# Optimization experiments

Hardware: AMD Instinct MI355X
Metric: run time of the kernel (lower is better)

## Reference

```python
import jax, jax.numpy as jnp
import numpy as np

M_STAGES = 10  # log2(1024)

def butterfly_mult_untied(twiddle, x, increasing_stride=True):
    """twiddle: (nstack, m, n//2, 2, 2); x: (batch, n) -> (batch, nstack*n)."""
    b, n = x.shape
    nstack, m = twiddle.shape[0], twiddle.shape[1]
    out = jnp.broadcast_to(x[:, None, :], (b, nstack, n))
    for block in range(m):
        log_stride = block if increasing_stride else (m - 1 - block)
        stride = 1 << log_stride
        # twiddle[:, log_stride] stores the factor for this stride
        t = twiddle[:, log_stride].reshape(nstack, n // (2 * stride), stride, 2, 2)
        o = out.reshape(b, nstack, n // (2 * stride), 2, stride)
        # new[b,k,g,i,s] = sum_j t[k,g,s,i,j] * o[b,k,g,j,s]
        out = jnp.einsum('kgsij,bkgjs->bkgis', t, o).reshape(b, nstack, n)
    return out.reshape(b, nstack * n)

def setup_inputs() -> dict:
    key = jax.random.key(0)
    k1, k2, k3 = jax.random.split(key, 3)
    in_size = 1024
    batch = 32768
    nstack = 1
    x = jax.random.normal(k1, (batch, in_size), dtype=jnp.float32)
    # non-ortho init: randn / sqrt(2)
    twiddle = jax.random.normal(k2, (nstack, M_STAGES, in_size // 2, 2, 2), dtype=jnp.float32) / np.sqrt(2.0).astype(np.float32)
    bound = 1.0 / np.sqrt(in_size)
    bias = jax.random.uniform(k3, (in_size,), dtype=jnp.float32, minval=-bound, maxval=bound)
    return {"x": x, "twiddle": twiddle, "bias": bias}

def reference(x, twiddle, bias):
    # in_size == in_size_extended == out_size (power of 2): no pad / mean / slice branches
    out = butterfly_mult_untied(twiddle, x, increasing_stride=True)
    return out + bias
```

## Files before the change

### kernel.cpp

```cpp
#include <hip/hip_runtime.h>


constexpr int ROWS  = 4;
constexpr int WAVES = 4;
constexpr int N     = 1024;

__device__ __forceinline__ void pair_update(float (&v)[ROWS][16], int s0, int s1,
                                            const float4 t4)
{
    #pragma unroll
    for (int r = 0; r < ROWS; ++r) {
        const float x0 = v[r][s0], x1 = v[r][s1];
        v[r][s0] = t4.x * x0 + t4.y * x1;
        v[r][s1] = t4.z * x0 + t4.w * x1;
    }
}

template<int LS>
__device__ __forceinline__ void cross_stage(float (&v)[ROWS][16],
                                            const float* __restrict__ tw,
                                            int lane)
{
    constexpr int m = 1 << (LS - 2);
    const int ipos = (lane >> (LS - 2)) & 1;
    const float* __restrict__ base = tw + LS * 2048;
    #pragma unroll
    for (int i = 0; i < 4; ++i) {
        #pragma unroll
        for (int j = 0; j < 4; ++j) {
            const int e    = i * 256 + lane * 4 + j;
            const int pair = ((e >> (LS + 1)) << LS) | (e & ((1 << LS) - 1));
            const float2 t2 = *reinterpret_cast<const float2*>(
                base + (size_t)pair * 4 + ipos * 2);
            const float ta = ipos ? t2.y : t2.x;
            const float tb = ipos ? t2.x : t2.y;
            const int s = i * 4 + j;
            #pragma unroll
            for (int r = 0; r < ROWS; ++r) {
                const float own  = v[r][s];
                const float part = __shfl_xor(own, m, 64);
                v[r][s] = ta * own + tb * part;
            }
        }
    }
}

__global__ __launch_bounds__(WAVES * 64)
void butterfly_kernel(const float* __restrict__ x,
                      const float* __restrict__ tw,
                      const float* __restrict__ bias,
                      float* __restrict__ out,
                      int batch)
{
    const int lane = (int)(threadIdx.x & 63u);
    const int wave = (int)(threadIdx.x >> 6u);
    const int row0 = (blockIdx.x * WAVES + wave) * ROWS;
    if (row0 >= batch) return;

    float v[ROWS][16];

    #pragma unroll
    for (int r = 0; r < ROWS; ++r) {
        const int row = (row0 + r < batch) ? (row0 + r) : (batch - 1);
        const float4* __restrict__ src =
            reinterpret_cast<const float4*>(x + (size_t)row * N);
        #pragma unroll
        for (int i = 0; i < 4; ++i) {
            const float4 t = src[i * 64 + lane];
            v[r][i*4+0] = t.x; v[r][i*4+1] = t.y;
            v[r][i*4+2] = t.z; v[r][i*4+3] = t.w;
        }
    }

    #pragma unroll
    for (int i = 0; i < 4; ++i) {
        #pragma unroll
        for (int jj = 0; jj < 2; ++jj) {
            const int pair = i * 128 + lane * 2 + jj;
            const float4 t4 = *reinterpret_cast<const float4*>(tw + (size_t)pair * 4);
            pair_update(v, i*4 + jj*2, i*4 + jj*2 + 1, t4);
        }
    }

    #pragma unroll
    for (int i = 0; i < 4; ++i) {
        #pragma unroll
        for (int j = 0; j < 2; ++j) {
            const int pair = i * 128 + lane * 2 + j;
            const float4 t4 = *reinterpret_cast<const float4*>(tw + 2048 + (size_t)pair * 4);
            pair_update(v, i*4 + j, i*4 + j + 2, t4);
        }
    }

    cross_stage<2>(v, tw, lane);
    cross_stage<3>(v, tw, lane);
    cross_stage<4>(v, tw, lane);
    cross_stage<5>(v, tw, lane);
    cross_stage<6>(v, tw, lane);
    cross_stage<7>(v, tw, lane);

    #pragma unroll
    for (int ih = 0; ih < 2; ++ih) {
        #pragma unroll
        for (int j = 0; j < 4; ++j) {
            const int pair = ih * 256 + lane * 4 + j;
            const float4 t4 = *reinterpret_cast<const float4*>(tw + 8*2048 + (size_t)pair * 4);
            pair_update(v, ih*8 + j, ih*8 + 4 + j, t4);
        }
    }

    #pragma unroll
    for (int i = 0; i < 2; ++i) {
        #pragma unroll
        for (int j = 0; j < 4; ++j) {
            const int pair = i * 256 + lane * 4 + j;
            const float4 t4 = *reinterpret_cast<const float4*>(tw + 9*2048 + (size_t)pair * 4);
            pair_update(v, i*4 + j, i*4 + 8 + j, t4);
        }
    }

    #pragma unroll
    for (int i = 0; i < 4; ++i) {
        const float4 b4 = *reinterpret_cast<const float4*>(bias + i * 256 + lane * 4);
        #pragma unroll
        for (int r = 0; r < ROWS; ++r) {
            if (row0 + r < batch) {
                float4 o;
                o.x = v[r][i*4+0] + b4.x;
                o.y = v[r][i*4+1] + b4.y;
                o.z = v[r][i*4+2] + b4.z;
                o.w = v[r][i*4+3] + b4.w;
                *reinterpret_cast<float4*>(out + (size_t)(row0 + r) * N + i * 256 + lane * 4) = o;
            }
        }
    }
}

extern "C" void kernel_launch(void* const* d_in, const int* in_sizes, int n_in,
                              void* d_out, int out_size, void* d_ws, size_t ws_size,
                              hipStream_t stream)
{
    (void)n_in; (void)d_ws; (void)ws_size; (void)out_size;
    const float* x    = (const float*)d_in[0];
    const float* tw   = (const float*)d_in[1];
    const float* bias = (const float*)d_in[2];
    float* out        = (float*)d_out;

    const int batch = in_sizes[0] / N;
    const int rows_per_block = WAVES * ROWS;
    const int blocks = (batch + rows_per_block - 1) / rows_per_block;
    hipLaunchKernelGGL(butterfly_kernel, dim3(blocks), dim3(WAVES * 64), 0, stream,
                       x, tw, bias, out, batch);
}
```

Before: 79.47 us.

## Transpose tile so each lane owns 64 contiguous columns of one row

Restructures the butterfly kernel so 1024-thread blocks process 64 rows, with each lane holding 64 consecutive columns of one row after an LDS transpose. The first six stages run fully in registers with wave-uniform (scalar) twiddle loads, and the last four stages exchange data between waves through swizzled LDS instead of lane shuffles. The aim is to remove the many cross-lane shuffles and per-lane twiddle gathers of the old layout. In exchange it adds many block-wide barriers, 64 KB of shared memory per block that limits occupancy, and heavy register pressure from 64 floats per thread.

After: 241.0 us. 203% more time.

```diff
diff --git a/kernel.cpp b/kernel.cpp
--- a/kernel.cpp
+++ b/kernel.cpp
@@ -1,137 +1,138 @@
 #include <hip/hip_runtime.h>
 
 
-constexpr int ROWS  = 4;
-constexpr int WAVES = 4;
-constexpr int N     = 1024;
+constexpr int N  = 1024;
+constexpr int TR = 64;
 
-__device__ __forceinline__ void pair_update(float (&v)[ROWS][16], int s0, int s1,
-                                            const float4 t4)
-{
-    #pragma unroll
-    for (int r = 0; r < ROWS; ++r) {
-        const float x0 = v[r][s0], x1 = v[r][s1];
-        v[r][s0] = t4.x * x0 + t4.y * x1;
-        v[r][s1] = t4.z * x0 + t4.w * x1;
-    }
-}
-
-template<int LS>
-__device__ __forceinline__ void cross_stage(float (&v)[ROWS][16],
-                                            const float* __restrict__ tw,
-                                            int lane)
-{
-    constexpr int m = 1 << (LS - 2);
-    const int ipos = (lane >> (LS - 2)) & 1;
-    const float* __restrict__ base = tw + LS * 2048;
-    #pragma unroll
-    for (int i = 0; i < 4; ++i) {
-        #pragma unroll
-        for (int j = 0; j < 4; ++j) {
-            const int e    = i * 256 + lane * 4 + j;
-            const int pair = ((e >> (LS + 1)) << LS) | (e & ((1 << LS) - 1));
-            const float2 t2 = *reinterpret_cast<const float2*>(
-                base + (size_t)pair * 4 + ipos * 2);
-            const float ta = ipos ? t2.y : t2.x;
-            const float tb = ipos ? t2.x : t2.y;
-            const int s = i * 4 + j;
-            #pragma unroll
-            for (int r = 0; r < ROWS; ++r) {
-                const float own  = v[r][s];
-                const float part = __shfl_xor(own, m, 64);
-                v[r][s] = ta * own + tb * part;
-            }
-        }
-    }
-}
-
-__global__ __launch_bounds__(WAVES * 64)
+__global__ __launch_bounds__(1024)
 void butterfly_kernel(const float* __restrict__ x,
                       const float* __restrict__ tw,
                       const float* __restrict__ bias,
                       float* __restrict__ out,
                       int batch)
 {
-    const int lane = (int)(threadIdx.x & 63u);
-    const int wave = (int)(threadIdx.x >> 6u);
-    const int row0 = (blockIdx.x * WAVES + wave) * ROWS;
-    if (row0 >= batch) return;
+    __shared__ __align__(16) float lds[16384];
 
-    float v[ROWS][16];
+    const int tid = (int)threadIdx.x;
+    const int l   = tid & 63;
+    const int w   = tid >> 6;
+    const int wu  = __builtin_amdgcn_readfirstlane(w);
+    const int row0 = (int)blockIdx.x * TR;
 
-    #pragma unroll
-    for (int r = 0; r < ROWS; ++r) {
-        const int row = (row0 + r < batch) ? (row0 + r) : (batch - 1);
-        const float4* __restrict__ src =
-            reinterpret_cast<const float4*>(x + (size_t)row * N);
+    float v[64];
+    float4* const ex = reinterpret_cast<float4*>(lds);
+
+    float4 tmp[4];
+    {
         #pragma unroll
-        for (int i = 0; i < 4; ++i) {
-            const float4 t = src[i * 64 + lane];
-            v[r][i*4+0] = t.x; v[r][i*4+1] = t.y;
-            v[r][i*4+2] = t.z; v[r][i*4+3] = t.w;
+        for (int kk = 0; kk < 4; ++kk) {
+            const int R = w * 4 + kk;
+            int row = row0 + R; if (row >= batch) row = batch - 1;
+            tmp[kk] = reinterpret_cast<const float4*>(x + (size_t)row * N)[l];
+        }
+        #pragma unroll
+        for (int s = 0; s < 4; ++s) {
+            __syncthreads();
+            #pragma unroll
+            for (int kk = 0; kk < 4; ++kk) {
+                const int R = w * 4 + kk;
+                ex[R * 64 + (l ^ (R & 7))] = tmp[kk];
+            }
+            __syncthreads();
+            if (s < 3) {
+                #pragma unroll
+                for (int kk = 0; kk < 4; ++kk) {
+                    const int R = w * 4 + kk;
+                    int row = row0 + R; if (row >= batch) row = batch - 1;
+                    tmp[kk] = reinterpret_cast<const float4*>(
+                        x + (size_t)row * N + (s + 1) * 256)[l];
+                }
+            }
+            if ((w >> 2) == s) {
+                #pragma unroll
+                for (int q = 0; q < 16; ++q) {
+                    const int quad = (w & 3) * 16 + q;
+                    const float4 t = ex[l * 64 + (quad ^ (l & 7))];
+                    v[q*4+0] = t.x; v[q*4+1] = t.y;
+                    v[q*4+2] = t.z; v[q*4+3] = t.w;
+                }
+            }
         }
     }
 
-    #pragma unroll
-    for (int i = 0; i < 4; ++i) {
-        #pragma unroll
-        for (int jj = 0; jj < 2; ++jj) {
-            const int pair = i * 128 + lane * 2 + jj;
-            const float4 t4 = *reinterpret_cast<const float4*>(tw + (size_t)pair * 4);
-            pair_update(v, i*4 + jj*2, i*4 + jj*2 + 1, t4);
-        }
+    #define INTH(LS)                                                         \
+    {                                                                        \
+        const int tb = (LS) * 2048 + wu * 128;                               \
+        _Pragma("unroll")                                                    \
+        for (int p = 0; p < 32; ++p) {                                       \
+            const int k0 = ((p >> (LS)) << ((LS) + 1)) | (p & ((1 << (LS)) - 1)); \
+            const int k1 = k0 + (1 << (LS));                                 \
+            const float t0 = tw[tb + p*4 + 0], t1 = tw[tb + p*4 + 1];        \
+            const float t2 = tw[tb + p*4 + 2], t3 = tw[tb + p*4 + 3];        \
+            const float a = v[k0], b = v[k1];                                \
+            v[k0] = t0 * a + t1 * b;                                         \
+            v[k1] = t2 * a + t3 * b;                                         \
+        }                                                                    \
     }
+    INTH(0) INTH(1) INTH(2) INTH(3) INTH(4) INTH(5)
+    #undef INTH
+
+    #define CROSS(LS, MASK)                                                  \
+    {                                                                        \
+        const int P0   = ((wu >> ((LS) - 5)) << (LS))                        \
+                       + (wu & ((1 << ((LS) - 6)) - 1)) * 64;                \
+        const int ipos = (wu >> ((LS) - 6)) & 1;                             \
+        const int tb   = (LS) * 2048 + P0 * 4;                               \
+        _Pragma("unroll")                                                    \
+        for (int sl = 0; sl < 4; ++sl) {                                     \
+            __syncthreads();                                                 \
+            _Pragma("unroll")                                                \
+            for (int Q = 0; Q < 4; ++Q) {                                    \
+                const int k = sl * 16 + Q * 4;                               \
+                ex[w * 256 + l * 4 + (Q ^ ((l >> 1) & 3))] =                 \
+                    make_float4(v[k], v[k+1], v[k+2], v[k+3]);               \
+            }                                                                \
+            __syncthreads();                                                 \
+            float4 pq[4];                                                    \
+            _Pragma("unroll")                                                \
+            for (int Q = 0; Q < 4; ++Q)                                      \
+                pq[Q] = ex[(w ^ (MASK)) * 256 + l * 4 + (Q ^ ((l >> 1) & 3))]; \
+            _Pragma("unroll")                                                \
+            for (int t = 0; t < 16; ++t) {                                   \
+                const int k = sl * 16 + t;                                   \
+                const float4 P = pq[t >> 2];                                 \
+                const float pa = (t & 3) == 0 ? P.x : (t & 3) == 1 ? P.y     \
+                               : (t & 3) == 2 ? P.z : P.w;                   \
+                const float co = tw[tb + k*4 + ipos*3];                      \
+                const float cp = tw[tb + k*4 + 1 + ipos];                    \
+                v[k] = co * v[k] + cp * pa;                                  \
+            }                                                                \
+        }                                                                    \
+    }
+    CROSS(6, 1) CROSS(7, 2) CROSS(8, 4) CROSS(9, 8)
+    #undef CROSS
 
     #pragma unroll
-    for (int i = 0; i < 4; ++i) {
-        #pragma unroll
-        for (int j = 0; j < 2; ++j) {
-            const int pair = i * 128 + lane * 2 + j;
-            const float4 t4 = *reinterpret_cast<const float4*>(tw + 2048 + (size_t)pair * 4);
-            pair_update(v, i*4 + j, i*4 + j + 2, t4);
-        }
-    }
-
-    cross_stage<2>(v, tw, lane);
-    cross_stage<3>(v, tw, lane);
-    cross_stage<4>(v, tw, lane);
-    cross_stage<5>(v, tw, lane);
-    cross_stage<6>(v, tw, lane);
-    cross_stage<7>(v, tw, lane);
+    for (int k = 0; k < 64; ++k) v[k] += bias[wu * 64 + k];
 
     #pragma unroll
-    for (int ih = 0; ih < 2; ++ih) {
+    for (int s = 0; s < 4; ++s) {
+        __syncthreads();
+        if ((w >> 2) == s) {
+            #pragma unroll
+            for (int q = 0; q < 16; ++q) {
+                const int quad = (w & 3) * 16 + q;
+                ex[l * 64 + (quad ^ (l & 7))] =
+                    make_float4(v[q*4], v[q*4+1], v[q*4+2], v[q*4+3]);
+            }
+        }
+        __syncthreads();
         #pragma unroll
-        for (int j = 0; j < 4; ++j) {
-            const int pair = ih * 256 + lane * 4 + j;
-            const float4 t4 = *reinterpret_cast<const float4*>(tw + 8*2048 + (size_t)pair * 4);
-            pair_update(v, ih*8 + j, ih*8 + 4 + j, t4);
-        }
-    }
-
-    #pragma unroll
-    for (int i = 0; i < 2; ++i) {
-        #pragma unroll
-        for (int j = 0; j < 4; ++j) {
-            const int pair = i * 256 + lane * 4 + j;
-            const float4 t4 = *reinterpret_cast<const float4*>(tw + 9*2048 + (size_t)pair * 4);
-            pair_update(v, i*4 + j, i*4 + 8 + j, t4);
-        }
-    }
-
-    #pragma unroll
-    for (int i = 0; i < 4; ++i) {
-        const float4 b4 = *reinterpret_cast<const float4*>(bias + i * 256 + lane * 4);
-        #pragma unroll
-        for (int r = 0; r < ROWS; ++r) {
-            if (row0 + r < batch) {
-                float4 o;
-                o.x = v[r][i*4+0] + b4.x;
-                o.y = v[r][i*4+1] + b4.y;
-                o.z = v[r][i*4+2] + b4.z;
-                o.w = v[r][i*4+3] + b4.w;
-                *reinterpret_cast<float4*>(out + (size_t)(row0 + r) * N + i * 256 + lane * 4) = o;
-            }
+        for (int kk = 0; kk < 4; ++kk) {
+            const int R = w * 4 + kk;
+            const float4 t = ex[R * 64 + (l ^ (R & 7))];
+            if (row0 + R < batch)
+                reinterpret_cast<float4*>(out + (size_t)(row0 + R) * N + s * 256)[l] = t;
         }
     }
 }
@@ -146,9 +147,8 @@
     const float* bias = (const float*)d_in[2];
     float* out        = (float*)d_out;
 
-    const int batch = in_sizes[0] / N;
-    const int rows_per_block = WAVES * ROWS;
-    const int blocks = (batch + rows_per_block - 1) / rows_per_block;
-    hipLaunchKernelGGL(butterfly_kernel, dim3(blocks), dim3(WAVES * 64), 0, stream,
+    const int batch  = in_sizes[0] / N;
+    const int blocks = (batch + TR - 1) / TR;
+    hipLaunchKernelGGL(butterfly_kernel, dim3(blocks), dim3(1024), 0, stream,
                        x, tw, bias, out, batch);
 }
```
